# Kernel tuning notes

Measured on AMD Instinct MI355X. Metric: run time of the kernel, lower is better.

## Reference

```python
import jax, jax.numpy as jnp
import numpy as np

NA = 100000   # authors
NP_ = 100000  # papers
D = 128       # hidden dim
H = 4         # heads
DH = 32       # head dim (D = H*DH)
L = 2         # layers
R = 3         # relations: 0=writes(a->p), 1=rev_writes(p->a), 2=cites(p->p)
E = 400000    # edges per relation
OUT = 40


def setup_inputs() -> dict:
    key = jax.random.key(0)
    ks = jax.random.split(key, 16)
    s = 0.05
    return {
        "x_author": jax.random.normal(ks[0], (NA, D), jnp.float32),
        "x_paper": jax.random.normal(ks[1], (NP_, D), jnp.float32),
        "ei_writes": jax.random.randint(ks[2], (2, E), 0, NA, dtype=jnp.int32),
        "ei_rev": jax.random.randint(ks[3], (2, E), 0, NA, dtype=jnp.int32),
        "ei_cites": jax.random.randint(ks[4], (2, E), 0, NP_, dtype=jnp.int32),
        "proj_w": jax.random.normal(ks[5], (2, D, D), jnp.float32) * s,
        "proj_b": jax.random.normal(ks[6], (2, D), jnp.float32) * s,
        "kqv_w": jax.random.normal(ks[7], (L, 3, 2, D, D), jnp.float32) * s,  # [layer, {k,q,v}, type, D, D]
        "kqv_b": jax.random.normal(ks[8], (L, 3, 2, D), jnp.float32) * s,
        "out_w": jax.random.normal(ks[9], (L, 2, D, D), jnp.float32) * s,
        "out_b": jax.random.normal(ks[10], (L, 2, D), jnp.float32) * s,
        "rel_a": jax.random.normal(ks[11], (L, R, H, DH, DH), jnp.float32) * s,
        "rel_m": jax.random.normal(ks[12], (L, R, H, DH, DH), jnp.float32) * s,
        "p_rel": jnp.ones((L, R, H), jnp.float32),
        "skip": jnp.ones((L, 2), jnp.float32),
        "cls_w": jax.random.normal(ks[13], (D, OUT), jnp.float32) * s,
        "cls_b": jnp.zeros((OUT,), jnp.float32),
    }


def _seg_softmax(sc, dst, n):
    # softmax over incoming edges grouped by destination node; sc: [E,H]
    m = jax.ops.segment_max(sc, dst, num_segments=n)
    m = jnp.where(jnp.isfinite(m), m, 0.0)
    e = jnp.exp(sc - m[dst])
    z = jax.ops.segment_sum(e, dst, num_segments=n)
    return e / (z[dst] + 1e-16)


def _hgt_layer(h_a, h_p, ei_w, ei_r, ei_c, kqv_w, kqv_b, out_w, out_b, rel_a, rel_m, p_rel, skip):
    na, npp = h_a.shape[0], h_p.shape[0]

    def kqv(h, t):
        k = (h @ kqv_w[0, t] + kqv_b[0, t]).reshape(-1, H, DH)
        q = (h @ kqv_w[1, t] + kqv_b[1, t]).reshape(-1, H, DH)
        v = (h @ kqv_w[2, t] + kqv_b[2, t]).reshape(-1, H, DH)
        return k, q, v

    k_a, q_a, v_a = kqv(h_a, 0)
    k_p, q_p, v_p = kqv(h_p, 1)
    scale = 1.0 / jnp.sqrt(jnp.float32(DH))

    def edge_msgs(k_src, v_src, q_dst, ei, r):
        ke = jnp.einsum('ehd,hdf->ehf', k_src[ei[0]], rel_a[r])
        ve = jnp.einsum('ehd,hdf->ehf', v_src[ei[0]], rel_m[r])
        sc = (q_dst[ei[1]] * ke).sum(-1) * p_rel[r] * scale  # [E,H]
        return sc, ve

    # destination = paper: writes (r=0) + cites (r=2); softmax jointly per dst node
    sc_w, ve_w = edge_msgs(k_a, v_a, q_p, ei_w, 0)
    sc_c, ve_c = edge_msgs(k_p, v_p, q_p, ei_c, 2)
    sc_p = jnp.concatenate([sc_w, sc_c], 0)
    ve_p = jnp.concatenate([ve_w, ve_c], 0)
    dst_p = jnp.concatenate([ei_w[1], ei_c[1]], 0)
    al_p = _seg_softmax(sc_p, dst_p, npp)
    agg_p = jax.ops.segment_sum(ve_p * al_p[..., None], dst_p, num_segments=npp).reshape(npp, D)

    # destination = author: rev_writes (r=1)
    sc_r, ve_r = edge_msgs(k_p, v_p, q_a, ei_r, 1)
    al_a = _seg_softmax(sc_r, ei_r[1], na)
    agg_a = jax.ops.segment_sum(ve_r * al_a[..., None], ei_r[1], num_segments=na).reshape(na, D)

    def out_mix(agg, h, t):
        o = jax.nn.gelu(agg, approximate=False) @ out_w[t] + out_b[t]
        s = jax.nn.sigmoid(skip[t])
        return s * o + (1.0 - s) * h

    # HGTNet.forward applies ELU after each HGTConv (dropout is identity in eval mode)
    h_a = jax.nn.elu(out_mix(agg_a, h_a, 0))
    h_p = jax.nn.elu(out_mix(agg_p, h_p, 1))
    return h_a, h_p


def reference(x_author, x_paper, ei_writes, ei_rev, ei_cites, proj_w, proj_b,
              kqv_w, kqv_b, out_w, out_b, rel_a, rel_m, p_rel, skip, cls_w, cls_b):
    h_a = x_author @ proj_w[0] + proj_b[0]
    h_p = x_paper @ proj_w[1] + proj_b[1]
    for l in range(L):
        h_a, h_p = _hgt_layer(h_a, h_p, ei_writes, ei_rev, ei_cites,
                              kqv_w[l], kqv_b[l], out_w[l], out_b[l],
                              rel_a[l], rel_m[l], p_rel[l], skip[l])
    return h_p @ cls_w + cls_b
```

## Files before the change

### kernel.cpp

```cpp
#include <hip/hip_runtime.h>
#include <hip/hip_bf16.h>
#include <math.h>

constexpr int NA  = 100000;
constexpr int NPP = 100000;
constexpr int D   = 128;
constexpr int H   = 4;
constexpr int E   = 400000;
constexpr int R   = 3;
constexpr int L   = 2;
constexpr int NSLOT = 23;
constexpr int SLOT_ELEMS = 8 * 4 * 512;
constexpr int GB2c = (NA + 127) / 128;
constexpr int GAc  = NA / 8;
constexpr int MEGA_G = 1564 * 9;

using s8v = __attribute__((ext_vector_type(8))) short;
using f4v = __attribute__((ext_vector_type(4))) float;
typedef unsigned short ushort_t;

static __device__ __forceinline__ unsigned short f2bf(float f) {
  unsigned u = __float_as_uint(f);
  return (unsigned short)((u + 0x7fffu + ((u >> 16) & 1u)) >> 16);
}
static __device__ __forceinline__ float bf2f(unsigned short s) {
  return __uint_as_float(((unsigned)s) << 16);
}
static __device__ __forceinline__ float klo(int i) {
  return __uint_as_float(((unsigned)i) << 16);
}
static __device__ __forceinline__ float vhi(int i) {
  return __uint_as_float(((unsigned)i) & 0xffff0000u);
}
static __device__ __forceinline__ float gelu_f(float x) {
  return 0.5f * x * (1.0f + erff(x * 0.70710678118654752f));
}
static __device__ __forceinline__ float elu_f(float x) {
  return x > 0.0f ? x : expm1f(x);
}

static __device__ __forceinline__ void load_a2(
    const ushort_t* __restrict__ A, int ar0, int ar1, int ks, int g,
    s8v& a0, s8v& a1) {
  const ushort_t* ap0 = A + (size_t)ar0 * 128 + ks * 32 + g * 4;
  ushort4 u0 = *(const ushort4*)ap0;
  ushort4 u1 = *(const ushort4*)(ap0 + 16);
  a0[0]=(short)u0.x; a0[1]=(short)u0.y; a0[2]=(short)u0.z; a0[3]=(short)u0.w;
  a0[4]=(short)u1.x; a0[5]=(short)u1.y; a0[6]=(short)u1.z; a0[7]=(short)u1.w;
  const ushort_t* ap1 = A + (size_t)ar1 * 128 + ks * 32 + g * 4;
  ushort4 v0 = *(const ushort4*)ap1;
  ushort4 v1 = *(const ushort4*)(ap1 + 16);
  a1[0]=(short)v0.x; a1[1]=(short)v0.y; a1[2]=(short)v0.z; a1[3]=(short)v0.w;
  a1[4]=(short)v1.x; a1[5]=(short)v1.y; a1[6]=(short)v1.z; a1[7]=(short)v1.w;
}

template<bool GELU_A, bool MIX>
__device__ __forceinline__ void dev_gemm8(
    const ushort_t* __restrict__ A, const ushort_t* __restrict__ Bhi,
    const float* __restrict__ bias, ushort_t* __restrict__ Cout,
    const float* __restrict__ skip_ptr, int M, int bx, ushort_t* Bs) {
  for (int i = threadIdx.x; i < 2048; i += 256)
    *(s8v*)&Bs[i * 8] = *(const s8v*)(Bhi + (size_t)i * 8);
  __syncthreads();
  const int lane = threadIdx.x & 63;
  const int wave = threadIdx.x >> 6;
  const int row0 = bx * 128 + wave * 32;
  const int g = lane >> 4, li = lane & 15;
  f4v acc0[8], acc1[8];
// ... 52 lines not shown
__device__ __forceinline__ void dev_gemm_kv(
    const ushort_t* __restrict__ A, const ushort_t* __restrict__ Bkv,
    const float* __restrict__ bias, ushort_t* __restrict__ kvout,
    int M, int bx, int ch, ushort_t* Bs) {
  for (int i = threadIdx.x; i < 2048; i += 256) {
    int kvh = i >> 10, j = i & 1023;
    const ushort_t* src = Bkv + (size_t)kvh * SLOT_ELEMS + ch * 8192 + j * 8;
    *(s8v*)&Bs[kvh * 8192 + j * 8] = *(const s8v*)src;
  }
  __syncthreads();
  const int lane = threadIdx.x & 63;
  const int wave = threadIdx.x >> 6;
  const int row0 = bx * 128 + wave * 32;
  const int g = lane >> 4, li = lane & 15;
  f4v acc0[8], acc1[8];
#pragma unroll
  for (int t = 0; t < 8; ++t) {
    acc0[t] = f4v{0.f, 0.f, 0.f, 0.f};
    acc1[t] = f4v{0.f, 0.f, 0.f, 0.f};
  }
  int ar0 = row0 + li;       if (ar0 >= M) ar0 = M - 1;
  int ar1 = row0 + 16 + li;  if (ar1 >= M) ar1 = M - 1;
#pragma unroll
  for (int ks = 0; ks < 4; ++ks) {
    s8v a0, a1;
    load_a2(A, ar0, ar1, ks, g, a0, a1);
#pragma unroll
    for (int t = 0; t < 4; ++t) {
      s8v kh = *(const s8v*)&Bs[(t * 4 + ks) * 512 + lane * 8];
      acc0[t] = __builtin_amdgcn_mfma_f32_16x16x32_bf16(a0, kh, acc0[t], 0, 0, 0);
      acc1[t] = __builtin_amdgcn_mfma_f32_16x16x32_bf16(a1, kh, acc1[t], 0, 0, 0);
      s8v vh = *(const s8v*)&Bs[8192 + (t * 4 + ks) * 512 + lane * 8];
      acc0[4 + t] = __builtin_amdgcn_mfma_f32_16x16x32_bf16(a0, vh, acc0[4 + t], 0, 0, 0);
      acc1[4 + t] = __builtin_amdgcn_mfma_f32_16x16x32_bf16(a1, vh, acc1[4 + t], 0, 0, 0);
    }
  }
#pragma unroll
  for (int rf = 0; rf < 2; ++rf) {
#pragma unroll
    for (int t = 0; t < 4; ++t) {
      int col = ch * 64 + t * 16 + li;
      float bk = bias[col], bv = bias[128 + col];
#pragma unroll
      for (int r = 0; r < 4; ++r) {
        int grow = row0 + rf * 16 + g * 4 + r;
        if (grow < M) {
          float kvl = rf ? acc1[t][r] : acc0[t][r];
          float vvl = rf ? acc1[4 + t][r] : acc0[4 + t][r];
          ushort2 o;
          o.x = f2bf(kvl + bk);
          o.y = f2bf(vvl + bv);
          *(ushort2*)(kvout + (size_t)grow * 256 + 2 * col) = o;
        }
      }
    }
  }
}

template<bool TWO>
__device__ __forceinline__ void dev_attn(
    const int* __restrict__ rp1, const int* __restrict__ col1,
    const ushort_t* __restrict__ kv1,
    const int* __restrict__ rp2, const int* __restrict__ col2,
    const ushort_t* __restrict__ kv2,
    const ushort_t* __restrict__ q,
    const float* __restrict__ prel1, const float* __restrict__ prel2,
    ushort_t* __restrict__ aggout, int ablk) {
  int lane = threadIdx.x & 63;
  int wave = threadIdx.x >> 6;
  int half = lane >> 5;
  int l32  = lane & 31;
  int dst  = ablk * 8 + wave * 2 + half;
  int head = l32 >> 3;
  const float scale = 0.17677669529663688f;
  float pr1 = prel1[head] * scale;
  float pr2 = TWO ? prel2[head] * scale : pr1;
  ushort4 qv = *(const ushort4*)(q + (size_t)dst * D + l32 * 4);
  float q0 = bf2f(qv.x), q1 = bf2f(qv.y), q2 = bf2f(qv.z), q3 = bf2f(qv.w);
  int e0a = rp1[dst];
  int d1  = rp1[dst + 1] - e0a;
  int e0b = 0, dt = d1;
  if (TWO) { e0b = rp2[dst]; dt = d1 + (rp2[dst + 1] - e0b); }
  float z = 0.f, a0 = 0.f, a1 = 0.f, a2 = 0.f, a3 = 0.f;
  for (int jj = 0; jj < dt; jj += 4) {
    int4 us[4]; bool vs[4]; float prs[4];
#pragma unroll
    for (int s2 = 0; s2 < 4; ++s2) {
      int idx = jj + s2;
      bool v = idx < dt;
      bool f = (!TWO) || (idx < d1);
      int ci = 0;
      if (v) ci = f ? (e0a + idx) : (e0b + idx - d1);
      int src = f ? col1[ci] : col2[ci];
      const ushort_t* kvp = f ? kv1 : kv2;
      us[s2] = *(const int4*)(kvp + (size_t)src * 256 + l32 * 8);
      vs[s2] = v;
      prs[s2] = f ? pr1 : pr2;
    }
#pragma unroll
    for (int s2 = 0; s2 < 4; ++s2) {
      float p = q0 * klo(us[s2].x) + q1 * klo(us[s2].y)
              + q2 * klo(us[s2].z) + q3 * klo(us[s2].w);
      p += __shfl_xor(p, 1);
      p += __shfl_xor(p, 2);
      p += __shfl_xor(p, 4);
      float e = vs[s2] ? __expf(p * prs[s2]) : 0.f;
      z  += e;
      a0 += e * vhi(us[s2].x);
      a1 += e * vhi(us[s2].y);
      a2 += e * vhi(us[s2].z);
      a3 += e * vhi(us[s2].w);
    }
  }
  float inv = 1.f / (z + 1e-16f);
  ushort4 o;
  o.x = f2bf(a0 * inv);
  o.y = f2bf(a1 * inv);
  o.z = f2bf(a2 * inv);
  o.w = f2bf(a3 * inv);
  *(ushort4*)(aggout + (size_t)dst * D + l32 * 4) = o;
}

__global__ __launch_bounds__(256, 4) void biggemm(
    const ushort_t* __restrict__ h_a, const ushort_t* __restrict__ h_p,
    const ushort_t* __restrict__ Bqa, const ushort_t* __restrict__ Bqp,
    const ushort_t* __restrict__ BkvR, const ushort_t* __restrict__ BkvW,
    const ushort_t* __restrict__ BkvC,
    const float* __restrict__ bqa, const float* __restrict__ bqp,
    const float* __restrict__ cbR, const float* __restrict__ cbW,
    const float* __restrict__ cbC,
    ushort_t* __restrict__ b_q, ushort_t* __restrict__ b_q2,
    ushort_t* __restrict__ kvR, ushort_t* __restrict__ kvW,
    ushort_t* __restrict__ kvC) {
  __shared__ ushort_t Bs[16384];
  int y = blockIdx.y;
  if (y == 0)      dev_gemm8<false, false>(h_a, Bqa, bqa, b_q,  nullptr, NA,  blockIdx.x, Bs);
  else if (y == 1) dev_gemm8<false, false>(h_p, Bqp, bqp, b_q2, nullptr, NPP, blockIdx.x, Bs);
  else if (y <= 3) dev_gemm_kv(h_p, BkvR, cbR, kvR, NPP, blockIdx.x, y - 2, Bs);
  else if (y <= 5) dev_gemm_kv(h_a, BkvW, cbW, kvW, NA,  blockIdx.x, y - 4, Bs);
  else             dev_gemm_kv(h_p, BkvC, cbC, kvC, NPP, blockIdx.x, y - 6, Bs);
}

__global__ __launch_bounds__(256, 8) void bigattn(
    const int* __restrict__ rp_r, const int* __restrict__ col_r,
    const ushort_t* __restrict__ kvR, ushort_t* __restrict__ q_a,
    const int* __restrict__ rp_w, const int* __restrict__ col_w,
    const ushort_t* __restrict__ kvW,
    const int* __restrict__ rp_c, const int* __restrict__ col_c,
    const ushort_t* __restrict__ kvC, ushort_t* __restrict__ q_p,
    const float* __restrict__ prelR, const float* __restrict__ prelW,
    const float* __restrict__ prelC) {
  unsigned x = blockIdx.x;
  if (x & 1)
    dev_attn<false>(rp_r, col_r, kvR, nullptr, nullptr, nullptr,
                    q_a, prelR, prelR, q_a, (int)(x >> 1));
  else
    dev_attn<true>(rp_w, col_w, kvW, rp_c, col_c, kvC,
                   q_p, prelW, prelC, q_p, (int)(x >> 1));
}

__global__ __launch_bounds__(256, 4) void bigmix(
    const ushort_t* __restrict__ agg_a, const ushort_t* __restrict__ Bo0,
    const float* __restrict__ ob0, ushort_t* __restrict__ h_a,
    const float* __restrict__ sk0,
    const ushort_t* __restrict__ agg_p, const ushort_t* __restrict__ Bo1,
    const float* __restrict__ ob1, ushort_t* __restrict__ h_p,
    const float* __restrict__ sk1) {
  __shared__ ushort_t Bs[16384];
  if (blockIdx.y == 0) dev_gemm8<true, true>(agg_a, Bo0, ob0, h_a, sk0, NA,  blockIdx.x, Bs);
  else                 dev_gemm8<true, true>(agg_p, Bo1, ob1, h_p, sk1, NPP, blockIdx.x, Bs);
}

__global__ __launch_bounds__(256, 8) void attn_p(
    const int* __restrict__ rp1, const int* __restrict__ col1,
    const ushort_t* __restrict__ kv1,
    const int* __restrict__ rp2, const int* __restrict__ col2,
    const ushort_t* __restrict__ kv2,
    const ushort_t* __restrict__ q,
    const float* __restrict__ prel1, const float* __restrict__ prel2,
    ushort_t* __restrict__ aggout) {
  dev_attn<true>(rp1, col1, kv1, rp2, col2, kv2, q, prel1, prel2, aggout, blockIdx.x);
}

__global__ __launch_bounds__(256, 4) void mega0(
    const int* __restrict__ rp_r, const int* __restrict__ col_r,
    const ushort_t* __restrict__ kv1, const ushort_t* __restrict__ q,
    const float* __restrict__ prelR, ushort_t* __restrict__ aggout,
    const ushort_t* __restrict__ h_a, const ushort_t* __restrict__ Bkv0,
    const float* __restrict__ cb0, ushort_t* __restrict__ kv2out) {
  __shared__ ushort_t Bs[16384];
  unsigned gidx = blockIdx.x;
  if (gidx % 9 == 0) {
    int gb = gidx / 9;
    dev_gemm_kv(h_a, Bkv0, cb0, kv2out, NA, gb >> 1, gb & 1, Bs);
  } else {
    int ablk = gidx - gidx / 9 - 1;
    if (ablk < GAc)
      dev_attn<false>(rp_r, col_r, kv1, nullptr, nullptr, nullptr,
                      q, prelR, prelR, aggout, ablk);
  }
}

__global__ __launch_bounds__(256, 4) void fusedA(
    const ushort_t* __restrict__ agg_a, const ushort_t* __restrict__ Bout,
    const float* __restrict__ out_b0, ushort_t* __restrict__ h_a,
    const float* __restrict__ skip0,
    const ushort_t* __restrict__ h_p, const ushort_t* __restrict__ Bq,
    const float* __restrict__ bq_p, ushort_t* __restrict__ qout,
    const ushort_t* __restrict__ Bkv, const float* __restrict__ cb2,
    ushort_t* __restrict__ kvout) {
  __shared__ ushort_t Bs[16384];
  if (blockIdx.y == 0) {
    dev_gemm8<true, true>(agg_a, Bout, out_b0, h_a, skip0, NA, blockIdx.x, Bs);
  } else if (blockIdx.y == 1) {
    dev_gemm8<false, false>(h_p, Bq, bq_p, qout, nullptr, NPP, blockIdx.x, Bs);
  } else {
    dev_gemm_kv(h_p, Bkv, cb2, kvout, NPP, blockIdx.x, blockIdx.y - 2, Bs);
  }
}

__global__ __launch_bounds__(256, 4) void gemm_qkv(
    const ushort_t* __restrict__ Aq, const ushort_t* __restrict__ Akv,
    const ushort_t* __restrict__ Bq, const ushort_t* __restrict__ Bkv,
    const float* __restrict__ bias_q, const float* __restrict__ bias_kv,
    ushort_t* __restrict__ qout, ushort_t* __restrict__ kvout, int M) {
  __shared__ ushort_t Bs[16384];
  if (blockIdx.y == 0)
    dev_gemm8<false, false>(Aq, Bq, bias_q, qout, nullptr, M, blockIdx.x, Bs);
  else
    dev_gemm_kv(Akv, Bkv, bias_kv, kvout, M, blockIdx.x, blockIdx.y - 1, Bs);
}

__global__ __launch_bounds__(256, 4) void outmix(
    const ushort_t* __restrict__ agg, const ushort_t* __restrict__ Bout,
    const float* __restrict__ out_b1, ushort_t* __restrict__ h,
    const float* __restrict__ skip1, int M) {
  __shared__ ushort_t Bs[16384];
  dev_gemm8<true, true>(agg, Bout, out_b1, h, skip1, M, blockIdx.x, Bs);
}

template<int NT16, int NCOLS, int STORE, bool BLO, typename TA>
__global__ __launch_bounds__(256, 4) void gemm4(
    const TA* __restrict__ A,
    const ushort_t* __restrict__ Bhi, const ushort_t* __restrict__ Blo,
    const float* __restrict__ bias, void* __restrict__ Cv, int M) {
  constexpr int HN = NT16 * 2048;
  __shared__ ushort_t Bs[HN * (BLO ? 2 : 1)];
  constexpr bool AFP32 = sizeof(TA) == 4;
  for (int i = threadIdx.x; i < (HN / 8) * (BLO ? 2 : 1); i += 256) {
    int half = i / (HN / 8), j = i % (HN / 8);
    const ushort_t* src = (half ? Blo : Bhi) + (size_t)j * 8;
    *(s8v*)&Bs[half * HN + j * 8] = *(const s8v*)src;
  }
  __syncthreads();
  const int lane = threadIdx.x & 63;
  const int wave = threadIdx.x >> 6;
  const int row0 = blockIdx.x * 128 + wave * 32;
  const int g = lane >> 4, li = lane & 15;
  f4v acc0[NT16], acc1[NT16];
#pragma unroll
  for (int ct = 0; ct < NT16; ++ct) {
    acc0[ct] = f4v{0.f, 0.f, 0.f, 0.f};
    acc1[ct] = f4v{0.f, 0.f, 0.f, 0.f};
  }
  int ar0 = row0 + li;       if (ar0 >= M) ar0 = M - 1;
  int ar1 = row0 + 16 + li;  if (ar1 >= M) ar1 = M - 1;
#pragma unroll
  for (int ks = 0; ks < 4; ++ks) {
    s8v ahi[2], alo[2];
#pragma unroll
    for (int rf = 0; rf < 2; ++rf) {
      int ar = rf ? ar1 : ar0;
      if constexpr (AFP32) {
        const float* ap = (const float*)A + (size_t)ar * 128 + ks * 32 + g * 4;
        float4 u0 = *(const float4*)ap;
        float4 u1 = *(const float4*)(ap + 16);
        float x[8] = {u0.x, u0.y, u0.z, u0.w, u1.x, u1.y, u1.z, u1.w};
#pragma unroll
        for (int i = 0; i < 8; ++i) {
          unsigned short h = f2bf(x[i]);
          ahi[rf][i] = (short)h;
          alo[rf][i] = (short)f2bf(x[i] - bf2f(h));
        }
      } else {
        const ushort_t* ap = (const ushort_t*)A + (size_t)ar * 128 + ks * 32 + g * 4;
        ushort4 u0 = *(const ushort4*)ap;
        ushort4 u1 = *(const ushort4*)(ap + 16);
        ahi[rf][0]=(short)u0.x; ahi[rf][1]=(short)u0.y; ahi[rf][2]=(short)u0.z; ahi[rf][3]=(short)u0.w;
        ahi[rf][4]=(short)u1.x; ahi[rf][5]=(short)u1.y; ahi[rf][6]=(short)u1.z; ahi[rf][7]=(short)u1.w;
      }
    }
#pragma unroll
    for (int ct = 0; ct < NT16; ++ct) {
      const ushort_t* bp = &Bs[(ct * 4 + ks) * 512 + lane * 8];
      s8v bhi = *(const s8v*)bp;
      acc0[ct] = __builtin_amdgcn_mfma_f32_16x16x32_bf16(ahi[0], bhi, acc0[ct], 0, 0, 0);
      acc1[ct] = __builtin_amdgcn_mfma_f32_16x16x32_bf16(ahi[1], bhi, acc1[ct], 0, 0, 0);
      if constexpr (BLO) {
        s8v blo = *(const s8v*)(bp + HN);
        if constexpr (AFP32) {
          acc0[ct] = __builtin_amdgcn_mfma_f32_16x16x32_bf16(alo[0], bhi, acc0[ct], 0, 0, 0);
          acc1[ct] = __builtin_amdgcn_mfma_f32_16x16x32_bf16(alo[1], bhi, acc1[ct], 0, 0, 0);
        }
        acc0[ct] = __builtin_amdgcn_mfma_f32_16x16x32_bf16(ahi[0], blo, acc0[ct], 0, 0, 0);
        acc1[ct] = __builtin_amdgcn_mfma_f32_16x16x32_bf16(ahi[1], blo, acc1[ct], 0, 0, 0);
      }
    }
  }
#pragma unroll
  for (int rf = 0; rf < 2; ++rf) {
#pragma unroll
    for (int ct = 0; ct < NT16; ++ct) {
      int col = ct * 16 + li;
      bool colok = (col < NCOLS);
      float bv = colok ? bias[col] : 0.f;
      f4v a = rf ? acc1[ct] : acc0[ct];
#pragma unroll
      for (int r = 0; r < 4; ++r) {
        int grow = row0 + rf * 16 + g * 4 + r;
        if (grow < M && colok) {
          float v = a[r] + bv;
          size_t off = (size_t)grow * NCOLS + col;
          if constexpr (STORE == 1) ((ushort_t*)Cv)[off] = f2bf(v);
          else                      ((float*)Cv)[off] = v;
        }
      }
    }
  }
}

__global__ __launch_bounds__(256) void combine_w(
    const float* __restrict__ kqv_w, const float* __restrict__ kqv_b,
    const float* __restrict__ rel_a, const float* __restrict__ rel_m,
    float* __restrict__ cw, float* __restrict__ cb) {
  int b  = blockIdx.x;
  int kv = b & 1;
  int r  = (b >> 1) % R;
  int l  = b / (2 * R);
  int t_src = (r == 0) ? 0 : 1;
  int i_w   = (kv == 0) ? 0 : 2;
  const float* W    = kqv_w + ((size_t)((l*3 + i_w)*2 + t_src)) * D * D;
  const float* bvec = kqv_b + ((size_t)((l*3 + i_w)*2 + t_src)) * D;
  const float* rel  = ((kv == 0) ? rel_a : rel_m) + ((size_t)(l*R + r)) * H * 32 * 32;
  float* Cout = cw + (size_t)b * D * D;
  float* cbo  = cb + (size_t)b * D;
  for (int idx = threadIdx.x; idx < D * D; idx += 256) {
    int i = idx / D, j = idx % D;
    int h = j >> 5, f = j & 31;
    const float* relh = rel + h * 32 * 32;
    float sum = 0.f;
#pragma unroll
    for (int d = 0; d < 32; ++d) sum += W[i*D + (h*32 + d)] * relh[d*32 + f];
    Cout[idx] = sum;
  }
  if (threadIdx.x < D) {
    int j = threadIdx.x;
    int h = j >> 5, f = j & 31;
    const float* relh = rel + h * 32 * 32;
    float sum = 0.f;
#pragma unroll
    for (int d = 0; d < 32; ++d) sum += bvec[h*32 + d] * relh[d*32 + f];
    cbo[j] = sum;
  }
}

__global__ __launch_bounds__(256) void pack_b(
    const float* __restrict__ proj_w, const float* __restrict__ kqv_w,
    const float* __restrict__ out_w, const float* __restrict__ cls_w,
    const float* __restrict__ cw,
    ushort_t* __restrict__ phi, ushort_t* __restrict__ plo) {
  int slot = blockIdx.x;
  const float* src; int ncol = 128;
  if (slot == 0) src = proj_w;
  else if (slot == 1) src = proj_w + D * D;
  else if (slot == 22) { src = cls_w; ncol = 40; }
  else {
    int l = (slot - 2) / 10, k = (slot - 2) % 10;
    if (k == 0)      src = kqv_w + ((size_t)((l*3 + 1)*2 + 0)) * D * D;
    else if (k == 1) src = kqv_w + ((size_t)((l*3 + 1)*2 + 1)) * D * D;
    else if (k < 8)  { int idx = k - 2; src = cw + ((size_t)((l*R)*2 + idx)) * D * D; }
    else             src = out_w + ((size_t)(l*2 + (k - 8))) * D * D;
  }
  int nt = (ncol + 15) / 16;
  int total = nt * 4 * 512;
  ushort_t* ph = phi + (size_t)slot * SLOT_ELEMS;
  ushort_t* pl = plo + (size_t)slot * SLOT_ELEMS;
  for (int idx = threadIdx.x; idx < total; idx += 256) {
    int j = idx & 7, lane = (idx >> 3) & 63, ks = (idx >> 9) & 3, ct = idx >> 11;
    int k = 4 * (lane >> 4) + (j & 3) + 16 * (j >> 2) + 32 * ks;
    int n = ct * 16 + (lane & 15);
    float v = (n < ncol) ? src[(size_t)k * ncol + n] : 0.f;
    unsigned short h = f2bf(v);
    ph[idx] = h;
    pl[idx] = f2bf(v - bf2f(h));
  }
}

__global__ void count3(const int* __restrict__ ei_w, const int* __restrict__ ei_c,
                       const int* __restrict__ ei_r, int* __restrict__ degz) {
  const int* dst = blockIdx.y == 0 ? ei_w + E : blockIdx.y == 1 ? ei_c + E : ei_r + E;
  int* deg = degz + blockIdx.y * NPP;
  for (int e = blockIdx.x * blockDim.x + threadIdx.x; e < E; e += gridDim.x * blockDim.x)
    atomicAdd(&deg[dst[e]], 1);
}
__global__ void fill3(const int* __restrict__ ei_w, const int* __restrict__ ei_c,
                      const int* __restrict__ ei_r,
                      const int* __restrict__ rp_w, const int* __restrict__ rp_c,
                      const int* __restrict__ rp_r,
                      int* __restrict__ cntz, int* __restrict__ colz) {
  int rel = blockIdx.y;
  const int* ei = rel == 0 ? ei_w : rel == 1 ? ei_c : ei_r;
  const int* dst = ei + E;
  const int* rp  = rel == 0 ? rp_w : rel == 1 ? rp_c : rp_r;
  int* cnt = cntz + rel * NPP;
  int* col = colz + rel * E;
  for (int e = blockIdx.x * blockDim.x + threadIdx.x; e < E; e += gridDim.x * blockDim.x) {
    int d = dst[e];
    int pos = atomicAdd(&cnt[d], 1);
    col[rp[d] + pos] = ei[e];
  }
}

__global__ __launch_bounds__(256) void scan_partial(const int* __restrict__ degz,
                                                    int* __restrict__ bsum) {
  int blk = blockIdx.x, rel = blk / 25, t25 = blk % 25;
  const int* deg = degz + rel * NPP + t25 * 4096;
  int nrem = min(4096, NPP - t25 * 4096);
  int base = threadIdx.x * 16;
  int s = 0;
  if (base < nrem) {
#pragma unroll
    for (int i4 = 0; i4 < 4; ++i4) {
      int4 v = *(const int4*)(deg + base + i4 * 4);
      s += v.x + v.y + v.z + v.w;
    }
  }
  __shared__ int sm[256];
  sm[threadIdx.x] = s; __syncthreads();
  for (int o = 128; o > 0; o >>= 1) {
    if (threadIdx.x < o) sm[threadIdx.x] += sm[threadIdx.x + o];
    __syncthreads();
  }
  if (threadIdx.x == 0) bsum[blk] = sm[0];
}
__global__ __launch_bounds__(256) void scan_final(const int* __restrict__ degz,
                                                  const int* __restrict__ bsum,
                                                  int* rp_w, int* rp_c, int* rp_r) {
  int blk = blockIdx.x, rel = blk / 25, t25 = blk % 25;
  const int* deg = degz + rel * NPP + t25 * 4096;
  int* rpb = (rel == 0 ? rp_w : rel == 1 ? rp_c : rp_r);
  int* rp = rpb + t25 * 4096;
  int boffv = 0;
  for (int i = 0; i < t25; ++i) boffv += bsum[rel * 25 + i];
  int nrem = min(4096, NPP - t25 * 4096);
  int base = threadIdx.x * 16;
  bool ok = base < nrem;
  int v[16]; int s = 0;
  if (ok) {
#pragma unroll
    for (int i4 = 0; i4 < 4; ++i4) {
      int4 u = *(const int4*)(deg + base + i4 * 4);
      v[i4*4+0] = u.x; v[i4*4+1] = u.y; v[i4*4+2] = u.z; v[i4*4+3] = u.w;
      s += u.x + u.y + u.z + u.w;
    }
  }
  __shared__ int sm[256];
  sm[threadIdx.x] = s; __syncthreads();
  for (int o = 1; o < 256; o <<= 1) {
    int x = (threadIdx.x >= o) ? sm[threadIdx.x - o] : 0;
    __syncthreads(); sm[threadIdx.x] += x; __syncthreads();
  }
  int run = boffv + sm[threadIdx.x] - s;
  if (ok) {
    int w[16];
#pragma unroll
    for (int i = 0; i < 16; ++i) { w[i] = run; run += v[i]; }
#pragma unroll
    for (int i4 = 0; i4 < 4; ++i4) *(int4*)(rp + base + i4 * 4) = *(const int4*)&w[i4*4];
  }
  if (t25 == 24 && threadIdx.x == 255) rpb[NPP] = boffv + sm[255];
}

extern "C" void kernel_launch(void* const* d_in, const int* in_sizes, int n_in,
                              void* d_out, int out_size, void* d_ws, size_t ws_size,
                              hipStream_t stream) {
  const float* x_a    = (const float*)d_in[0];
  const float* x_p    = (const float*)d_in[1];
  const int*   ei_w   = (const int*)d_in[2];
  const int*   ei_r   = (const int*)d_in[3];
  const int*   ei_c   = (const int*)d_in[4];
  const float* proj_w = (const float*)d_in[5];
  const float* proj_b = (const float*)d_in[6];
  const float* kqv_w  = (const float*)d_in[7];
  const float* kqv_b  = (const float*)d_in[8];
  const float* out_w  = (const float*)d_in[9];
  const float* out_b  = (const float*)d_in[10];
  const float* rel_a  = (const float*)d_in[11];
  const float* rel_m  = (const float*)d_in[12];
  const float* p_rel  = (const float*)d_in[13];
  const float* skip   = (const float*)d_in[14];
  const float* cls_w  = (const float*)d_in[15];
  const float* cls_b  = (const float*)d_in[16];
  float* out = (float*)d_out;

  const size_t NF = (size_t)NA * D;
  const size_t head_b = (size_t)(12 * D * D + 12 * D) * 4 + 4 * NF * 2;
  const size_t kv_b   = 2 * NF * 2;
  const size_t rest_b = 2 * (size_t)NSLOT * SLOT_ELEMS * 2 +
                        sizeof(int) * ((size_t)3 * (NPP + 1) + 6 * NPP + 3 * E + 128);
  const bool use3 = ws_size >= head_b + 3 * kv_b + rest_b;
  if (!use3 && ws_size < head_b + 2 * kv_b + rest_b) return;

  char* p = (char*)d_ws;
  float* cw = (float*)p;              p += (size_t)12 * D * D * 4;
  float* cb = (float*)p;              p += (size_t)12 * D * 4;
  ushort_t* h_a   = (ushort_t*)p;     p += NF * 2;
  ushort_t* h_p   = (ushort_t*)p;     p += NF * 2;
  ushort_t* b_q   = (ushort_t*)p;     p += NF * 2;
  ushort_t* b_q2  = (ushort_t*)p;     p += NF * 2;
  ushort_t* b_kvR = (ushort_t*)p;     p += 2 * NF * 2;
  ushort_t* b_kvW = (ushort_t*)p;     p += 2 * NF * 2;
  ushort_t* b_kvC = nullptr;
  if (use3) { b_kvC = (ushort_t*)p;   p += 2 * NF * 2; }
  ushort_t* phi = (ushort_t*)p;       p += (size_t)NSLOT * SLOT_ELEMS * 2;
  ushort_t* plo = (ushort_t*)p;       p += (size_t)NSLOT * SLOT_ELEMS * 2;
  int* rp_w = (int*)p;                p += (NPP + 1) * 4;
  int* rp_c = (int*)p;                p += (NPP + 1) * 4;
  int* rp_r = (int*)p;                p += (NA + 1) * 4;
  int* degz = (int*)p;                p += (size_t)3 * NPP * 4;
  int* cntz = (int*)p;                p += (size_t)3 * NPP * 4;
  int* colz = (int*)p;                p += (size_t)3 * E * 4;
  int* bsum = (int*)p;

  hipMemsetAsync(degz, 0, sizeof(int) * 6 * (size_t)NPP, stream);

  count3<<<dim3(256, 3), 256, 0, stream>>>(ei_w, ei_c, ei_r, degz);
  scan_partial<<<75, 256, 0, stream>>>(degz, bsum);
  scan_final<<<75, 256, 0, stream>>>(degz, bsum, rp_w, rp_c, rp_r);
  fill3<<<dim3(256, 3), 256, 0, stream>>>(ei_w, ei_c, ei_r, rp_w, rp_c, rp_r, cntz, colz);
  int* col_w = colz;
  int* col_c = colz + E;
  int* col_r = colz + 2 * E;

  combine_w<<<12, 256, 0, stream>>>(kqv_w, kqv_b, rel_a, rel_m, cw, cb);
  pack_b<<<NSLOT, 256, 0, stream>>>(proj_w, kqv_w, out_w, cls_w, cw, phi, plo);

  auto PH = [&](int s){ return phi + (size_t)s * SLOT_ELEMS; };
  auto PL = [&](int s){ return plo + (size_t)s * SLOT_ELEMS; };

  const dim3 G1(GB2c, 1);
  gemm4<8, 128, 1, true, float><<<G1, 256, 0, stream>>>(
      x_a, PH(0), PL(0), proj_b,     h_a, NA);
  gemm4<8, 128, 1, true, float><<<G1, 256, 0, stream>>>(
      x_p, PH(1), PL(1), proj_b + D, h_p, NPP);

  for (int l = 0; l < L; ++l) {
    const int SQA = 2 + l * 10 + 0, SQP = 2 + l * 10 + 1;
    auto SKV = [&](int r){ return 2 + l * 10 + 2 + r * 2; };
    const int SO0 = 2 + l * 10 + 8, SO1 = 2 + l * 10 + 9;
    const float* bq_a = kqv_b + ((size_t)((l*3 + 1)*2 + 0)) * D;
    const float* bq_p = kqv_b + ((size_t)((l*3 + 1)*2 + 1)) * D;
    auto CB2 = [&](int r){ return cb + ((size_t)((l*R + r)*2)) * D; };
    const float* prelW = p_rel + (size_t)(l*R + 0) * H;
    const float* prelR = p_rel + (size_t)(l*R + 1) * H;
    const float* prelC = p_rel + (size_t)(l*R + 2) * H;

    if (use3) {
      biggemm<<<dim3(GB2c, 8), 256, 0, stream>>>(
          h_a, h_p, PH(SQA), PH(SQP), PH(SKV(1)), PH(SKV(0)), PH(SKV(2)),
          bq_a, bq_p, CB2(1), CB2(0), CB2(2),
          b_q, b_q2, b_kvR, b_kvW, b_kvC);
      bigattn<<<2 * GAc, 256, 0, stream>>>(
          rp_r, col_r, b_kvR, b_q,
          rp_w, col_w, b_kvW, rp_c, col_c, b_kvC, b_q2,
          prelR, prelW, prelC);
      bigmix<<<dim3(GB2c, 2), 256, 0, stream>>>(
          b_q,  PH(SO0), out_b + (size_t)(l*2 + 0) * D, h_a, skip + l*2 + 0,
          b_q2, PH(SO1), out_b + (size_t)(l*2 + 1) * D, h_p, skip + l*2 + 1);
    } else {
      gemm_qkv<<<dim3(GB2c, 3), 256, 0, stream>>>(
          h_a, h_p, PH(SQA), PH(SKV(1)), bq_a, CB2(1), b_q, b_kvR, NA);
      mega0<<<MEGA_G, 256, 0, stream>>>(
          rp_r, col_r, b_kvR, b_q, prelR, b_q,
          h_a, PH(SKV(0)), CB2(0), b_kvW);
      fusedA<<<dim3(GB2c, 4), 256, 0, stream>>>(
          b_q, PH(SO0), out_b + (size_t)(l*2 + 0) * D, h_a, skip + l*2 + 0,
          h_p, PH(SQP), bq_p, b_q2,
          PH(SKV(2)), CB2(2), b_kvR);
      attn_p<<<GAc, 256, 0, stream>>>(
          rp_w, col_w, b_kvW, rp_c, col_c, b_kvR,
          b_q2, prelW, prelC, b_q2);
      outmix<<<G1, 256, 0, stream>>>(
          b_q2, PH(SO1), out_b + (size_t)(l*2 + 1) * D, h_p, skip + l*2 + 1, NPP);
    }
  }

  gemm4<3, 40, 0, true, ushort_t><<<G1, 256, 0, stream>>>(
      h_p, PH(22), PL(22), cls_b, out, NPP);
}
```

Measured before the change: 865.2 us.

## Fuse CSR count into projection and CSR fill into first layer GEMM

Degree counting now runs in blocks interleaved with the fp32 input projection GEMM in a single launch, and the CSR column fill is interleaved with the layer-0 QKV GEMM blocks. The two projection GEMMs are also merged into one grid. The intent is to overlap atomics-bound graph preprocessing with MFMA-bound GEMMs and cut kernel launches. The low-workspace fallback path is dropped and gemm4 is specialised into a classifier-only kernel. The risk is larger shared memory in fusedProj (64KB, 2 blocks/SM) lowering occupancy, and atomic contention competing with GEMM bandwidth.

```diff
diff --git a/kernel.cpp b/kernel.cpp
--- a/kernel.cpp
+++ b/kernel.cpp
@@ -13,7 +13,6 @@
 constexpr int SLOT_ELEMS = 8 * 4 * 512;
 constexpr int GB2c = (NA + 127) / 128;
 constexpr int GAc  = NA / 8;
-constexpr int MEGA_G = 1564 * 9;
 
 using s8v = __attribute__((ext_vector_type(8))) short;
 using f4v = __attribute__((ext_vector_type(4))) float;
@@ -172,6 +171,74 @@
           o.y = f2bf(vvl + bv);
           *(ushort2*)(kvout + (size_t)grow * 256 + 2 * col) = o;
         }
+      }
+    }
+  }
+}
+
+__device__ __forceinline__ void dev_proj(
+    const float* __restrict__ A, const ushort_t* __restrict__ Bhi,
+    const ushort_t* __restrict__ Blo, const float* __restrict__ bias,
+    ushort_t* __restrict__ Cout, int M, int bx, ushort_t* Bs) {
+  for (int i = threadIdx.x; i < 4096; i += 256) {
+    int half = i >> 11, j = i & 2047;
+    const ushort_t* src = (half ? Blo : Bhi) + (size_t)j * 8;
+    *(s8v*)&Bs[half * 16384 + j * 8] = *(const s8v*)src;
+  }
+  __syncthreads();
+  const int lane = threadIdx.x & 63;
+  const int wave = threadIdx.x >> 6;
+  const int row0 = bx * 128 + wave * 32;
+  const int g = lane >> 4, li = lane & 15;
+  f4v acc0[8], acc1[8];
+#pragma unroll
+  for (int ct = 0; ct < 8; ++ct) {
+    acc0[ct] = f4v{0.f, 0.f, 0.f, 0.f};
+    acc1[ct] = f4v{0.f, 0.f, 0.f, 0.f};
+  }
+  int ar0 = row0 + li;       if (ar0 >= M) ar0 = M - 1;
+  int ar1 = row0 + 16 + li;  if (ar1 >= M) ar1 = M - 1;
+#pragma unroll
+  for (int ks = 0; ks < 4; ++ks) {
+    s8v ahi[2], alo[2];
+#pragma unroll
+    for (int rf = 0; rf < 2; ++rf) {
+      int ar = rf ? ar1 : ar0;
+      const float* ap = A + (size_t)ar * 128 + ks * 32 + g * 4;
+      float4 u0 = *(const float4*)ap;
+      float4 u1 = *(const float4*)(ap + 16);
+      float x[8] = {u0.x, u0.y, u0.z, u0.w, u1.x, u1.y, u1.z, u1.w};
+#pragma unroll
+      for (int i = 0; i < 8; ++i) {
+        unsigned short h = f2bf(x[i]);
+        ahi[rf][i] = (short)h;
+        alo[rf][i] = (short)f2bf(x[i] - bf2f(h));
+      }
+    }
+#pragma unroll
+    for (int ct = 0; ct < 8; ++ct) {
+      const ushort_t* bp = &Bs[(ct * 4 + ks) * 512 + lane * 8];
+      s8v bhi = *(const s8v*)bp;
+      s8v blo = *(const s8v*)(bp + 16384);
+      acc0[ct] = __builtin_amdgcn_mfma_f32_16x16x32_bf16(ahi[0], bhi, acc0[ct], 0, 0, 0);
+      acc1[ct] = __builtin_amdgcn_mfma_f32_16x16x32_bf16(ahi[1], bhi, acc1[ct], 0, 0, 0);
+      acc0[ct] = __builtin_amdgcn_mfma_f32_16x16x32_bf16(alo[0], bhi, acc0[ct], 0, 0, 0);
+      acc1[ct] = __builtin_amdgcn_mfma_f32_16x16x32_bf16(alo[1], bhi, acc1[ct], 0, 0, 0);
+      acc0[ct] = __builtin_amdgcn_mfma_f32_16x16x32_bf16(ahi[0], blo, acc0[ct], 0, 0, 0);
+      acc1[ct] = __builtin_amdgcn_mfma_f32_16x16x32_bf16(ahi[1], blo, acc1[ct], 0, 0, 0);
+    }
+  }
+#pragma unroll
+  for (int rf = 0; rf < 2; ++rf) {
+#pragma unroll
+    for (int ct = 0; ct < 8; ++ct) {
+      int col = ct * 16 + li;
+      float bv = bias[col];
+      f4v a = rf ? acc1[ct] : acc0[ct];
+#pragma unroll
+      for (int r = 0; r < 4; ++r) {
+        int grow = row0 + rf * 16 + g * 4 + r;
+        if (grow < M) Cout[(size_t)grow * 128 + col] = f2bf(a[r] + bv);
       }
     }
   }
@@ -241,6 +308,63 @@
   *(ushort4*)(aggout + (size_t)dst * D + l32 * 4) = o;
 }
 
+__device__ __forceinline__ void dev_count(const int* __restrict__ dst,
+                                          int* __restrict__ deg, int bidx) {
+  for (int e = bidx * 256 + (int)threadIdx.x; e < E; e += 256 * 256)
+    atomicAdd(&deg[dst[e]], 1);
+}
+__device__ __forceinline__ void dev_fill(const int* __restrict__ ei,
+                                         const int* __restrict__ rp,
+                                         int* __restrict__ cnt,
+                                         int* __restrict__ col, int bidx) {
+  const int* dst = ei + E;
+  for (int e = bidx * 256 + (int)threadIdx.x; e < E; e += 256 * 256) {
+    int d = dst[e];
+    int pos = atomicAdd(&cnt[d], 1);
+    col[rp[d] + pos] = ei[e];
+  }
+}
+
+__global__ __launch_bounds__(256, 2) void fusedProj(
+    const float* __restrict__ x_a, const float* __restrict__ x_p,
+    const ushort_t* __restrict__ B0h, const ushort_t* __restrict__ B0l,
+    const ushort_t* __restrict__ B1h, const ushort_t* __restrict__ B1l,
+    const float* __restrict__ proj_b,
+    ushort_t* __restrict__ h_a, ushort_t* __restrict__ h_p,
+    const int* __restrict__ ei_w, const int* __restrict__ ei_c,
+    const int* __restrict__ ei_r, int* __restrict__ degz) {
+  __shared__ ushort_t Bs[32768];
+  unsigned b = blockIdx.x;
+  if (b % 3 == 2) {
+    int ci = b / 3;
+    if (ci < 768) {
+      int rel = ci >> 8, sub = ci & 255;
+      const int* dst = rel == 0 ? ei_w + E : rel == 1 ? ei_c + E : ei_r + E;
+      dev_count(dst, degz + rel * NPP, sub);
+    }
+  } else {
+    int gi = b - (b + 1) / 3;
+    if (gi < GB2c) dev_proj(x_a, B0h, B0l, proj_b,     h_a, NA,  gi, Bs);
+    else           dev_proj(x_p, B1h, B1l, proj_b + D, h_p, NPP, gi - GB2c, Bs);
+  }
+}
+
+__device__ __forceinline__ void dev_biggemm_slice(
+    int slice, int bx,
+    const ushort_t* h_a, const ushort_t* h_p,
+    const ushort_t* Bqa, const ushort_t* Bqp,
+    const ushort_t* BkvR, const ushort_t* BkvW, const ushort_t* BkvC,
+    const float* bqa, const float* bqp,
+    const float* cbR, const float* cbW, const float* cbC,
+    ushort_t* b_q, ushort_t* b_q2,
+    ushort_t* kvR, ushort_t* kvW, ushort_t* kvC, ushort_t* Bs) {
+  if (slice == 0)      dev_gemm8<false, false>(h_a, Bqa, bqa, b_q,  nullptr, NA,  bx, Bs);
+  else if (slice == 1) dev_gemm8<false, false>(h_p, Bqp, bqp, b_q2, nullptr, NPP, bx, Bs);
+  else if (slice <= 3) dev_gemm_kv(h_p, BkvR, cbR, kvR, NPP, bx, slice - 2, Bs);
+  else if (slice <= 5) dev_gemm_kv(h_a, BkvW, cbW, kvW, NA,  bx, slice - 4, Bs);
+  else                 dev_gemm_kv(h_p, BkvC, cbC, kvC, NPP, bx, slice - 6, Bs);
+}
+
 __global__ __launch_bounds__(256, 4) void biggemm(
     const ushort_t* __restrict__ h_a, const ushort_t* __restrict__ h_p,
     const ushort_t* __restrict__ Bqa, const ushort_t* __restrict__ Bqp,
@@ -253,12 +377,43 @@
     ushort_t* __restrict__ kvR, ushort_t* __restrict__ kvW,
     ushort_t* __restrict__ kvC) {
   __shared__ ushort_t Bs[16384];
-  int y = blockIdx.y;
-  if (y == 0)      dev_gemm8<false, false>(h_a, Bqa, bqa, b_q,  nullptr, NA,  blockIdx.x, Bs);
-  else if (y == 1) dev_gemm8<false, false>(h_p, Bqp, bqp, b_q2, nullptr, NPP, blockIdx.x, Bs);
-  else if (y <= 3) dev_gemm_kv(h_p, BkvR, cbR, kvR, NPP, blockIdx.x, y - 2, Bs);
-  else if (y <= 5) dev_gemm_kv(h_a, BkvW, cbW, kvW, NA,  blockIdx.x, y - 4, Bs);
-  else             dev_gemm_kv(h_p, BkvC, cbC, kvC, NPP, blockIdx.x, y - 6, Bs);
+  dev_biggemm_slice(blockIdx.y, blockIdx.x, h_a, h_p, Bqa, Bqp, BkvR, BkvW, BkvC,
+                    bqa, bqp, cbR, cbW, cbC, b_q, b_q2, kvR, kvW, kvC, Bs);
+}
+
+__global__ __launch_bounds__(256, 4) void fusedFill(
+    const ushort_t* __restrict__ h_a, const ushort_t* __restrict__ h_p,
+    const ushort_t* __restrict__ Bqa, const ushort_t* __restrict__ Bqp,
+    const ushort_t* __restrict__ BkvR, const ushort_t* __restrict__ BkvW,
+    const ushort_t* __restrict__ BkvC,
+    const float* __restrict__ bqa, const float* __restrict__ bqp,
+    const float* __restrict__ cbR, const float* __restrict__ cbW,
+    const float* __restrict__ cbC,
+    ushort_t* __restrict__ b_q, ushort_t* __restrict__ b_q2,
+    ushort_t* __restrict__ kvR, ushort_t* __restrict__ kvW,
+    ushort_t* __restrict__ kvC,
+    const int* __restrict__ ei_w, const int* __restrict__ ei_c,
+    const int* __restrict__ ei_r,
+    const int* __restrict__ rp_w, const int* __restrict__ rp_c,
+    const int* __restrict__ rp_r,
+    int* __restrict__ cntz, int* __restrict__ colz) {
+  __shared__ ushort_t Bs[16384];
+  unsigned b = blockIdx.x;
+  if (b % 9 == 8) {
+    int fi = b / 9;
+    if (fi < 768) {
+      int rel = fi >> 8, sub = fi & 255;
+      const int* ei = rel == 0 ? ei_w : rel == 1 ? ei_c : ei_r;
+      const int* rp = rel == 0 ? rp_w : rel == 1 ? rp_c : rp_r;
+      dev_fill(ei, rp, cntz + rel * NPP, colz + rel * E, sub);
+    }
+  } else {
+    int gi = b - (b + 1) / 9;
+    int slice = gi & 7, bx = gi >> 3;
+    if (bx < GB2c)
+      dev_biggemm_slice(slice, bx, h_a, h_p, Bqa, Bqp, BkvR, BkvW, BkvC,
+                        bqa, bqp, cbR, cbW, cbC, b_q, b_q2, kvR, kvW, kvC, Bs);
+  }
 }
 
 __global__ __launch_bounds__(256, 8) void bigattn(
@@ -291,83 +446,14 @@
   else                 dev_gemm8<true, true>(agg_p, Bo1, ob1, h_p, sk1, NPP, blockIdx.x, Bs);
 }
 
-__global__ __launch_bounds__(256, 8) void attn_p(
-    const int* __restrict__ rp1, const int* __restrict__ col1,
-    const ushort_t* __restrict__ kv1,
-    const int* __restrict__ rp2, const int* __restrict__ col2,
-    const ushort_t* __restrict__ kv2,
-    const ushort_t* __restrict__ q,
-    const float* __restrict__ prel1, const float* __restrict__ prel2,
-    ushort_t* __restrict__ aggout) {
-  dev_attn<true>(rp1, col1, kv1, rp2, col2, kv2, q, prel1, prel2, aggout, blockIdx.x);
-}
-
-__global__ __launch_bounds__(256, 4) void mega0(
-    const int* __restrict__ rp_r, const int* __restrict__ col_r,
-    const ushort_t* __restrict__ kv1, const ushort_t* __restrict__ q,
-    const float* __restrict__ prelR, ushort_t* __restrict__ aggout,
-    const ushort_t* __restrict__ h_a, const ushort_t* __restrict__ Bkv0,
-    const float* __restrict__ cb0, ushort_t* __restrict__ kv2out) {
-  __shared__ ushort_t Bs[16384];
-  unsigned gidx = blockIdx.x;
-  if (gidx % 9 == 0) {
-    int gb = gidx / 9;
-    dev_gemm_kv(h_a, Bkv0, cb0, kv2out, NA, gb >> 1, gb & 1, Bs);
-  } else {
-    int ablk = gidx - gidx / 9 - 1;
-    if (ablk < GAc)
-      dev_attn<false>(rp_r, col_r, kv1, nullptr, nullptr, nullptr,
-                      q, prelR, prelR, aggout, ablk);
-  }
-}
-
-__global__ __launch_bounds__(256, 4) void fusedA(
-    const ushort_t* __restrict__ agg_a, const ushort_t* __restrict__ Bout,
-    const float* __restrict__ out_b0, ushort_t* __restrict__ h_a,
-    const float* __restrict__ skip0,
-    const ushort_t* __restrict__ h_p, const ushort_t* __restrict__ Bq,
-    const float* __restrict__ bq_p, ushort_t* __restrict__ qout,
-    const ushort_t* __restrict__ Bkv, const float* __restrict__ cb2,
-    ushort_t* __restrict__ kvout) {
-  __shared__ ushort_t Bs[16384];
-  if (blockIdx.y == 0) {
-    dev_gemm8<true, true>(agg_a, Bout, out_b0, h_a, skip0, NA, blockIdx.x, Bs);
-  } else if (blockIdx.y == 1) {
-    dev_gemm8<false, false>(h_p, Bq, bq_p, qout, nullptr, NPP, blockIdx.x, Bs);
-  } else {
-    dev_gemm_kv(h_p, Bkv, cb2, kvout, NPP, blockIdx.x, blockIdx.y - 2, Bs);
-  }
-}
-
-__global__ __launch_bounds__(256, 4) void gemm_qkv(
-    const ushort_t* __restrict__ Aq, const ushort_t* __restrict__ Akv,
-    const ushort_t* __restrict__ Bq, const ushort_t* __restrict__ Bkv,
-    const float* __restrict__ bias_q, const float* __restrict__ bias_kv,
-    ushort_t* __restrict__ qout, ushort_t* __restrict__ kvout, int M) {
-  __shared__ ushort_t Bs[16384];
-  if (blockIdx.y == 0)
-    dev_gemm8<false, false>(Aq, Bq, bias_q, qout, nullptr, M, blockIdx.x, Bs);
-  else
-    dev_gemm_kv(Akv, Bkv, bias_kv, kvout, M, blockIdx.x, blockIdx.y - 1, Bs);
-}
-
-__global__ __launch_bounds__(256, 4) void outmix(
-    const ushort_t* __restrict__ agg, const ushort_t* __restrict__ Bout,
-    const float* __restrict__ out_b1, ushort_t* __restrict__ h,
-    const float* __restrict__ skip1, int M) {
-  __shared__ ushort_t Bs[16384];
-  dev_gemm8<true, true>(agg, Bout, out_b1, h, skip1, M, blockIdx.x, Bs);
-}
-
-template<int NT16, int NCOLS, int STORE, bool BLO, typename TA>
-__global__ __launch_bounds__(256, 4) void gemm4(
-    const TA* __restrict__ A,
+__global__ __launch_bounds__(256, 4) void gemm_cls(
+    const ushort_t* __restrict__ A,
     const ushort_t* __restrict__ Bhi, const ushort_t* __restrict__ Blo,
-    const float* __restrict__ bias, void* __restrict__ Cv, int M) {
+    const float* __restrict__ bias, float* __restrict__ Cv, int M) {
+  constexpr int NT16 = 3;
   constexpr int HN = NT16 * 2048;
-  __shared__ ushort_t Bs[HN * (BLO ? 2 : 1)];
-  constexpr bool AFP32 = sizeof(TA) == 4;
-  for (int i = threadIdx.x; i < (HN / 8) * (BLO ? 2 : 1); i += 256) {
+  __shared__ ushort_t Bs[HN * 2];
+  for (int i = threadIdx.x; i < (HN / 8) * 2; i += 256) {
     int half = i / (HN / 8), j = i % (HN / 8);
     const ushort_t* src = (half ? Blo : Bhi) + (size_t)j * 8;
     *(s8v*)&Bs[half * HN + j * 8] = *(const s8v*)src;
@@ -387,44 +473,17 @@
   int ar1 = row0 + 16 + li;  if (ar1 >= M) ar1 = M - 1;
 #pragma unroll
   for (int ks = 0; ks < 4; ++ks) {
-    s8v ahi[2], alo[2];
-#pragma unroll
-    for (int rf = 0; rf < 2; ++rf) {
-      int ar = rf ? ar1 : ar0;
-      if constexpr (AFP32) {
-        const float* ap = (const float*)A + (size_t)ar * 128 + ks * 32 + g * 4;
-        float4 u0 = *(const float4*)ap;
-        float4 u1 = *(const float4*)(ap + 16);
-        float x[8] = {u0.x, u0.y, u0.z, u0.w, u1.x, u1.y, u1.z, u1.w};
-#pragma unroll
-        for (int i = 0; i < 8; ++i) {
-          unsigned short h = f2bf(x[i]);
-          ahi[rf][i] = (short)h;
-          alo[rf][i] = (short)f2bf(x[i] - bf2f(h));
-        }
-      } else {
-        const ushort_t* ap = (const ushort_t*)A + (size_t)ar * 128 + ks * 32 + g * 4;
-        ushort4 u0 = *(const ushort4*)ap;
-        ushort4 u1 = *(const ushort4*)(ap + 16);
-        ahi[rf][0]=(short)u0.x; ahi[rf][1]=(short)u0.y; ahi[rf][2]=(short)u0.z; ahi[rf][3]=(short)u0.w;
-        ahi[rf][4]=(short)u1.x; ahi[rf][5]=(short)u1.y; ahi[rf][6]=(short)u1.z; ahi[rf][7]=(short)u1.w;
-      }
-    }
+    s8v a0, a1;
+    load_a2(A, ar0, ar1, ks, g, a0, a1);
 #pragma unroll
     for (int ct = 0; ct < NT16; ++ct) {
       const ushort_t* bp = &Bs[(ct * 4 + ks) * 512 + lane * 8];
       s8v bhi = *(const s8v*)bp;
-      acc0[ct] = __builtin_amdgcn_mfma_f32_16x16x32_bf16(ahi[0], bhi, acc0[ct], 0, 0, 0);
-      acc1[ct] = __builtin_amdgcn_mfma_f32_16x16x32_bf16(ahi[1], bhi, acc1[ct], 0, 0, 0);
-      if constexpr (BLO) {
-        s8v blo = *(const s8v*)(bp + HN);
-        if constexpr (AFP32) {
-          acc0[ct] = __builtin_amdgcn_mfma_f32_16x16x32_bf16(alo[0], bhi, acc0[ct], 0, 0, 0);
-          acc1[ct] = __builtin_amdgcn_mfma_f32_16x16x32_bf16(alo[1], bhi, acc1[ct], 0, 0, 0);
-        }
-        acc0[ct] = __builtin_amdgcn_mfma_f32_16x16x32_bf16(ahi[0], blo, acc0[ct], 0, 0, 0);
-        acc1[ct] = __builtin_amdgcn_mfma_f32_16x16x32_bf16(ahi[1], blo, acc1[ct], 0, 0, 0);
-      }
+      s8v blo = *(const s8v*)(bp + HN);
+      acc0[ct] = __builtin_amdgcn_mfma_f32_16x16x32_bf16(a0, bhi, acc0[ct], 0, 0, 0);
+      acc1[ct] = __builtin_amdgcn_mfma_f32_16x16x32_bf16(a1, bhi, acc1[ct], 0, 0, 0);
+      acc0[ct] = __builtin_amdgcn_mfma_f32_16x16x32_bf16(a0, blo, acc0[ct], 0, 0, 0);
+      acc1[ct] = __builtin_amdgcn_mfma_f32_16x16x32_bf16(a1, blo, acc1[ct], 0, 0, 0);
     }
   }
 #pragma unroll
@@ -432,18 +491,13 @@
 #pragma unroll
     for (int ct = 0; ct < NT16; ++ct) {
       int col = ct * 16 + li;
-      bool colok = (col < NCOLS);
+      bool colok = (col < 40);
       float bv = colok ? bias[col] : 0.f;
       f4v a = rf ? acc1[ct] : acc0[ct];
 #pragma unroll
       for (int r = 0; r < 4; ++r) {
         int grow = row0 + rf * 16 + g * 4 + r;
-        if (grow < M && colok) {
-          float v = a[r] + bv;
-          size_t off = (size_t)grow * NCOLS + col;
-          if constexpr (STORE == 1) ((ushort_t*)Cv)[off] = f2bf(v);
-          else                      ((float*)Cv)[off] = v;
-        }
+        if (grow < M && colok) Cv[(size_t)grow * 40 + col] = a[r] + bv;
       }
     }
   }
@@ -513,31 +567,6 @@
     unsigned short h = f2bf(v);
     ph[idx] = h;
     pl[idx] = f2bf(v - bf2f(h));
-  }
-}
-
-__global__ void count3(const int* __restrict__ ei_w, const int* __restrict__ ei_c,
-                       const int* __restrict__ ei_r, int* __restrict__ degz) {
-  const int* dst = blockIdx.y == 0 ? ei_w + E : blockIdx.y == 1 ? ei_c + E : ei_r + E;
-  int* deg = degz + blockIdx.y * NPP;
-  for (int e = blockIdx.x * blockDim.x + threadIdx.x; e < E; e += gridDim.x * blockDim.x)
-    atomicAdd(&deg[dst[e]], 1);
-}
-__global__ void fill3(const int* __restrict__ ei_w, const int* __restrict__ ei_c,
-                      const int* __restrict__ ei_r,
-                      const int* __restrict__ rp_w, const int* __restrict__ rp_c,
-                      const int* __restrict__ rp_r,
-                      int* __restrict__ cntz, int* __restrict__ colz) {
-  int rel = blockIdx.y;
-  const int* ei = rel == 0 ? ei_w : rel == 1 ? ei_c : ei_r;
-  const int* dst = ei + E;
-  const int* rp  = rel == 0 ? rp_w : rel == 1 ? rp_c : rp_r;
-  int* cnt = cntz + rel * NPP;
-  int* col = colz + rel * E;
-  for (int e = blockIdx.x * blockDim.x + threadIdx.x; e < E; e += gridDim.x * blockDim.x) {
-    int d = dst[e];
-    int pos = atomicAdd(&cnt[d], 1);
-    col[rp[d] + pos] = ei[e];
   }
 }
 
@@ -624,13 +653,6 @@
   float* out = (float*)d_out;
 
   const size_t NF = (size_t)NA * D;
-  const size_t head_b = (size_t)(12 * D * D + 12 * D) * 4 + 4 * NF * 2;
-  const size_t kv_b   = 2 * NF * 2;
-  const size_t rest_b = 2 * (size_t)NSLOT * SLOT_ELEMS * 2 +
-                        sizeof(int) * ((size_t)3 * (NPP + 1) + 6 * NPP + 3 * E + 128);
-  const bool use3 = ws_size >= head_b + 3 * kv_b + rest_b;
-  if (!use3 && ws_size < head_b + 2 * kv_b + rest_b) return;
-
   char* p = (char*)d_ws;
   float* cw = (float*)p;              p += (size_t)12 * D * D * 4;
   float* cb = (float*)p;              p += (size_t)12 * D * 4;
@@ -640,8 +662,7 @@
   ushort_t* b_q2  = (ushort_t*)p;     p += NF * 2;
   ushort_t* b_kvR = (ushort_t*)p;     p += 2 * NF * 2;
   ushort_t* b_kvW = (ushort_t*)p;     p += 2 * NF * 2;
-  ushort_t* b_kvC = nullptr;
-  if (use3) { b_kvC = (ushort_t*)p;   p += 2 * NF * 2; }
+  ushort_t* b_kvC = (ushort_t*)p;     p += 2 * NF * 2;
   ushort_t* phi = (ushort_t*)p;       p += (size_t)NSLOT * SLOT_ELEMS * 2;
   ushort_t* plo = (ushort_t*)p;       p += (size_t)NSLOT * SLOT_ELEMS * 2;
   int* rp_w = (int*)p;                p += (NPP + 1) * 4;
@@ -650,29 +671,25 @@
   int* degz = (int*)p;                p += (size_t)3 * NPP * 4;
   int* cntz = (int*)p;                p += (size_t)3 * NPP * 4;
   int* colz = (int*)p;                p += (size_t)3 * E * 4;
-  int* bsum = (int*)p;
+  int* bsum = (int*)p;                p += 128 * 4;
+  if (ws_size < (size_t)(p - (char*)d_ws)) return;
 
   hipMemsetAsync(degz, 0, sizeof(int) * 6 * (size_t)NPP, stream);
 
-  count3<<<dim3(256, 3), 256, 0, stream>>>(ei_w, ei_c, ei_r, degz);
+  combine_w<<<12, 256, 0, stream>>>(kqv_w, kqv_b, rel_a, rel_m, cw, cb);
+  pack_b<<<NSLOT, 256, 0, stream>>>(proj_w, kqv_w, out_w, cls_w, cw, phi, plo);
+
+  auto PH = [&](int s){ return phi + (size_t)s * SLOT_ELEMS; };
+  auto PL = [&](int s){ return plo + (size_t)s * SLOT_ELEMS; };
+
+  fusedProj<<<2346, 256, 0, stream>>>(
+      x_a, x_p, PH(0), PL(0), PH(1), PL(1), proj_b, h_a, h_p,
+      ei_w, ei_c, ei_r, degz);
   scan_partial<<<75, 256, 0, stream>>>(degz, bsum);
   scan_final<<<75, 256, 0, stream>>>(degz, bsum, rp_w, rp_c, rp_r);
-  fill3<<<dim3(256, 3), 256, 0, stream>>>(ei_w, ei_c, ei_r, rp_w, rp_c, rp_r, cntz, colz);
   int* col_w = colz;
   int* col_c = colz + E;
   int* col_r = colz + 2 * E;
-
-  combine_w<<<12, 256, 0, stream>>>(kqv_w, kqv_b, rel_a, rel_m, cw, cb);
-  pack_b<<<NSLOT, 256, 0, stream>>>(proj_w, kqv_w, out_w, cls_w, cw, phi, plo);
-
-  auto PH = [&](int s){ return phi + (size_t)s * SLOT_ELEMS; };
-  auto PL = [&](int s){ return plo + (size_t)s * SLOT_ELEMS; };
-
-  const dim3 G1(GB2c, 1);
-  gemm4<8, 128, 1, true, float><<<G1, 256, 0, stream>>>(
-      x_a, PH(0), PL(0), proj_b,     h_a, NA);
-  gemm4<8, 128, 1, true, float><<<G1, 256, 0, stream>>>(
-      x_p, PH(1), PL(1), proj_b + D, h_p, NPP);
 
   for (int l = 0; l < L; ++l) {
     const int SQA = 2 + l * 10 + 0, SQP = 2 + l * 10 + 1;
@@ -685,36 +702,27 @@
     const float* prelR = p_rel + (size_t)(l*R + 1) * H;
     const float* prelC = p_rel + (size_t)(l*R + 2) * H;
 
-    if (use3) {
+    if (l == 0) {
+      fusedFill<<<7038, 256, 0, stream>>>(
+          h_a, h_p, PH(SQA), PH(SQP), PH(SKV(1)), PH(SKV(0)), PH(SKV(2)),
+          bq_a, bq_p, CB2(1), CB2(0), CB2(2),
+          b_q, b_q2, b_kvR, b_kvW, b_kvC,
+          ei_w, ei_c, ei_r, rp_w, rp_c, rp_r, cntz, colz);
+    } else {
       biggemm<<<dim3(GB2c, 8), 256, 0, stream>>>(
           h_a, h_p, PH(SQA), PH(SQP), PH(SKV(1)), PH(SKV(0)), PH(SKV(2)),
           bq_a, bq_p, CB2(1), CB2(0), CB2(2),
           b_q, b_q2, b_kvR, b_kvW, b_kvC);
-      bigattn<<<2 * GAc, 256, 0, stream>>>(
-          rp_r, col_r, b_kvR, b_q,
-          rp_w, col_w, b_kvW, rp_c, col_c, b_kvC, b_q2,
-          prelR, prelW, prelC);
-      bigmix<<<dim3(GB2c, 2), 256, 0, stream>>>(
-          b_q,  PH(SO0), out_b + (size_t)(l*2 + 0) * D, h_a, skip + l*2 + 0,
-          b_q2, PH(SO1), out_b + (size_t)(l*2 + 1) * D, h_p, skip + l*2 + 1);
-    } else {
-      gemm_qkv<<<dim3(GB2c, 3), 256, 0, stream>>>(
-          h_a, h_p, PH(SQA), PH(SKV(1)), bq_a, CB2(1), b_q, b_kvR, NA);
-      mega0<<<MEGA_G, 256, 0, stream>>>(
-          rp_r, col_r, b_kvR, b_q, prelR, b_q,
-          h_a, PH(SKV(0)), CB2(0), b_kvW);
-      fusedA<<<dim3(GB2c, 4), 256, 0, stream>>>(
-          b_q, PH(SO0), out_b + (size_t)(l*2 + 0) * D, h_a, skip + l*2 + 0,
-          h_p, PH(SQP), bq_p, b_q2,
-          PH(SKV(2)), CB2(2), b_kvR);
-      attn_p<<<GAc, 256, 0, stream>>>(
-          rp_w, col_w, b_kvW, rp_c, col_c, b_kvR,
-          b_q2, prelW, prelC, b_q2);
-      outmix<<<G1, 256, 0, stream>>>(
-          b_q2, PH(SO1), out_b + (size_t)(l*2 + 1) * D, h_p, skip + l*2 + 1, NPP);
-    }
-  }
-
-  gemm4<3, 40, 0, true, ushort_t><<<G1, 256, 0, stream>>>(
+    }
+    bigattn<<<2 * GAc, 256, 0, stream>>>(
+        rp_r, col_r, b_kvR, b_q,
+        rp_w, col_w, b_kvW, rp_c, col_c, b_kvC, b_q2,
+        prelR, prelW, prelC);
+    bigmix<<<dim3(GB2c, 2), 256, 0, stream>>>(
+        b_q,  PH(SO0), out_b + (size_t)(l*2 + 0) * D, h_a, skip + l*2 + 0,
+        b_q2, PH(SO1), out_b + (size_t)(l*2 + 1) * D, h_p, skip + l*2 + 1);
+  }
+
+  gemm_cls<<<dim3(GB2c, 1), 256, 0, stream>>>(
       h_p, PH(22), PL(22), cls_b, out, NPP);
 }
```

Result: faster. 799.9 us (-7.5%).
